# Performance work log

Measured on AMD Instinct MI355X. Metric: run time of the kernel, lower is better.

Reference implementation:

```python
import jax, jax.numpy as jnp
import numpy as np

N = 50000      # nodes
F_IN = 128     # num_feat
HID = 128      # hidden size
OUT = 47       # num_out (classes)
E = 600000     # graph edges
EGO_E = 1200000  # concatenated egonet edges


def _linear_params(key, fan_in, fan_out):
    s = 1.0 / np.sqrt(fan_in)
    kw, kb = jax.random.split(key)
    W = jax.random.uniform(kw, (fan_in, fan_out), jnp.float32, -s, s)
    b = jax.random.uniform(kb, (fan_out,), jnp.float32, -s, s)
    return W, b


def setup_inputs() -> dict:
    key = jax.random.key(0)
    ks = jax.random.split(key, 8)
    x_in = jax.random.normal(ks[0], (N, F_IN), jnp.float32)
    edge_index_in = jax.random.randint(ks[1], (2, E), 0, N)
    ego_edge_index = jax.random.randint(ks[2], (2, EGO_E), 0, N)
    W_ego0, b_ego0 = _linear_params(ks[3], F_IN, F_IN)
    W_gin0, b_gin0 = _linear_params(ks[4], F_IN, HID)
    W_ego1, b_ego1 = _linear_params(ks[5], HID, HID)
    W_gin1, b_gin1 = _linear_params(ks[6], HID, OUT)
    return {
        "x_in": x_in, "edge_index_in": edge_index_in, "ego_edge_index": ego_edge_index,
        "W_ego0": W_ego0, "b_ego0": b_ego0, "W_gin0": W_gin0, "b_gin0": b_gin0,
        "W_ego1": W_ego1, "b_ego1": b_ego1, "W_gin1": W_gin1, "b_gin1": b_gin1,
    }


def reference(x_in, edge_index_in, ego_edge_index,
              W_ego0, b_ego0, W_gin0, b_gin0,
              W_ego1, b_ego1, W_gin1, b_gin1):
    n = x_in.shape[0]
    ego_row, ego_col = ego_edge_index[0], ego_edge_index[1]
    src, tgt = edge_index_in[0], edge_index_in[1]

    def do_conv(x):
        # sum_i spmm(A_i, x) == scatter-add over concatenated egonet edges, then / N
        return jax.ops.segment_sum(x[ego_col], ego_row, num_segments=n) * (1.0 / n)

    def gin(x, W, b):
        # GINConv(nn=Linear), eps=0: Linear(x + sum_{j->i} x_j)
        aggr = jax.ops.segment_sum(x[src], tgt, num_segments=n)
        return (x + aggr) @ W + b

    # layer 0: ['Ego','GIN', relu_mid=True, relu_end=True]
    x = do_conv(x_in) @ W_ego0 + b_ego0
    x = jax.nn.relu(x)
    x = gin(x, W_gin0, b_gin0)
    x = jax.nn.relu(x)
    # layer 1: ['Ego','GIN', relu_mid=True, relu_end=False]
    x = do_conv(x) @ W_ego1 + b_ego1
    x = jax.nn.relu(x)
    x = gin(x, W_gin1, b_gin1)
    return jax.nn.log_softmax(x, axis=1)
```

## Files before the change

### kernel.cpp

```cpp
#include <hip/hip_runtime.h>

#define SCAP_EGO 8192
#define SCAP_E   4096

typedef unsigned short ushort_t;
typedef unsigned int uint_t;
typedef __attribute__((ext_vector_type(8))) short bf16x8;
typedef __attribute__((ext_vector_type(4))) float f32x4;

__device__ inline float lo16(uint_t u) { return __uint_as_float(u << 16); }
__device__ inline float hi16(uint_t u) { return __uint_as_float(u & 0xFFFF0000u); }
__device__ inline ushort_t f2bf(float f) {
    uint_t i = __float_as_uint(f);
    return (ushort_t)((i + 0x7FFFu + ((i >> 16) & 1u)) >> 16);
}
__device__ inline uint_t pack2(float a, float b) {
    return (uint_t)f2bf(a) | ((uint_t)f2bf(b) << 16);
}
union U8 { uint4 u; bf16x8 v; };

__global__ __launch_bounds__(256) void prep(
    const float* __restrict__ x, ushort_t* __restrict__ xb, int n8,
    const float* __restrict__ W0, const float* __restrict__ W1,
    const float* __restrict__ W2, const float* __restrict__ W3,
    ushort_t* __restrict__ T0, ushort_t* __restrict__ T1,
    ushort_t* __restrict__ T2, ushort_t* __restrict__ T3,
    int* __restrict__ z)
{
    int i = blockIdx.x * 256 + threadIdx.x;
    if (i < 128) ((int4*)z)[i] = make_int4(0, 0, 0, 0);
    if (i < n8) {
        const float4* p = (const float4*)(x + (size_t)i * 8);
        float4 a = p[0], b = p[1];
        uint4 o;
        o.x = pack2(a.x, a.y); o.y = pack2(a.z, a.w);
        o.z = pack2(b.x, b.y); o.w = pack2(b.z, b.w);
        *(uint4*)(xb + (size_t)i * 8) = o;
    }
    if (i < 49152) {
        int mi = i >> 14;
        int r = i & 16383;
        int n = r >> 7, k = r & 127;
        const float* W = mi == 0 ? W0 : (mi == 1 ? W1 : W2);
        ushort_t* T = mi == 0 ? T0 : (mi == 1 ? T1 : T2);
        T[n * 128 + k] = f2bf(W[k * 128 + n]);
    } else if (i < 49152 + 6144) {
        int r = i - 49152;
        int n = r >> 7, k = r & 127;
        T3[n * 128 + k] = (n < 47) ? f2bf(W3[k * 47 + n]) : (ushort_t)0;
    }
}

__global__ __launch_bounds__(256) void bin_edges2(
    const int* __restrict__ d1, const int* __restrict__ s1, int n1, int nb1,
    int* __restrict__ cur1, int2* __restrict__ st1, int scap1,
    const int* __restrict__ d2, const int* __restrict__ s2, int n2,
    int* __restrict__ cur2, int2* __restrict__ st2, int scap2)
{
    const int* dst; const int* src; int nE, scap; int* bincur; int2* stage; int bid;
    if (blockIdx.x < (uint_t)nb1) {
        dst = d1; src = s1; nE = n1; scap = scap1; bincur = cur1; stage = st1;
        bid = blockIdx.x;
    } else {
        dst = d2; src = s2; nE = n2; scap = scap2; bincur = cur2; stage = st2;
        bid = blockIdx.x - nb1;
    }
    __shared__ int bcnt[256];
    __shared__ int gbase[256];
    int t = threadIdx.x;
    bcnt[t] = 0;
    __syncthreads();
    int base = bid * 4096;
    int d[16], s[16], l[16];
#pragma unroll
    for (int i = 0; i < 16; i++) {
        int e = base + t + i * 256;
        if (e < nE) {
            d[i] = dst[e]; s[i] = src[e];
            l[i] = atomicAdd(&bcnt[d[i] >> 8], 1);
        } else d[i] = -1;
    }
    __syncthreads();
    if (bcnt[t]) gbase[t] = atomicAdd(&bincur[t], bcnt[t]);
    __syncthreads();
#pragma unroll
    for (int i = 0; i < 16; i++) {
        if (d[i] >= 0) {
            int b = d[i] >> 8;
            int slot = gbase[b] + l[i];
            if (slot < scap) stage[(size_t)b * scap + slot] = make_int2(d[i], s[i]);
        }
    }
}

__global__ __launch_bounds__(256) void build_csr2(
    const int* __restrict__ cur1, const int2* __restrict__ st1, int scap1,
    int* __restrict__ cnt1, int* __restrict__ rp1, int* __restrict__ pk1,
    const int* __restrict__ cur2, const int2* __restrict__ st2, int scap2,
    int* __restrict__ cnt2, int* __restrict__ rp2, int* __restrict__ pk2,
    int NB)
{
    const int* bincur; const int2* stage; int scap;
    int* cnt; int* rowptr; int* packed; int b;
    if (blockIdx.x < (uint_t)NB) {
        bincur = cur1; stage = st1; scap = scap1;
        cnt = cnt1; rowptr = rp1; packed = pk1; b = blockIdx.x;
    } else {
        bincur = cur2; stage = st2; scap = scap2;
        cnt = cnt2; rowptr = rp2; packed = pk2; b = blockIdx.x - NB;
    }
    __shared__ int sc[256];
    __shared__ int wcur[256];
    int t = threadIdx.x;
    int m = bincur[b]; if (m > scap) m = scap;
    const int2* st = stage + (size_t)b * scap;
    sc[t] = 0;
    __syncthreads();
    for (int e = t; e < m; e += 256) atomicAdd(&sc[st[e].x & 255], 1);
    __syncthreads();
    int v = sc[t];
    __syncthreads();
    sc[t] = v;
    __syncthreads();
    for (int off = 1; off < 256; off <<= 1) {
        int y = (t >= off) ? sc[t - off] : 0;
        __syncthreads();
        sc[t] += y;
        __syncthreads();
    }
    int excl = sc[t] - v;
    cnt[b * 256 + t] = v;
    rowptr[b * 256 + t] = b * scap + excl;
    wcur[t] = excl;
    __syncthreads();
    int* pk = packed + (size_t)b * scap;
    for (int e = t; e < m; e += 256) {
        int2 p = st[e];
        int slot = atomicAdd(&wcur[p.x & 255], 1);
        pk[slot] = p.y;
    }
}

__global__ __launch_bounds__(256) void gather_bf(
    const ushort_t* __restrict__ x, const int* __restrict__ cnt,
    const int* __restrict__ rowptr, const int* __restrict__ packed,
    ushort_t* __restrict__ outb, int nNodes, float scale, int selfAdd)
{
    int g = threadIdx.x >> 4, lane = threadIdx.x & 15;
    int n = blockIdx.x * 16 + g;
    if (n >= nNodes) return;
    int len = cnt[n];
    const int* row = packed + rowptr[n];
    const ushort_t* base = x + lane * 8;
    float a[8];
#pragma unroll
    for (int m = 0; m < 8; m++) a[m] = 0.f;
    int e = 0;
    for (; e + 3 < len; e += 4) {
        int s0 = row[e], s1 = row[e + 1], s2 = row[e + 2], s3 = row[e + 3];
        uint4 w0 = *(const uint4*)(base + (size_t)s0 * 128);
        uint4 w1 = *(const uint4*)(base + (size_t)s1 * 128);
        uint4 w2 = *(const uint4*)(base + (size_t)s2 * 128);
        uint4 w3 = *(const uint4*)(base + (size_t)s3 * 128);
        a[0] += lo16(w0.x) + lo16(w1.x) + lo16(w2.x) + lo16(w3.x);
        a[1] += hi16(w0.x) + hi16(w1.x) + hi16(w2.x) + hi16(w3.x);
        a[2] += lo16(w0.y) + lo16(w1.y) + lo16(w2.y) + lo16(w3.y);
        a[3] += hi16(w0.y) + hi16(w1.y) + hi16(w2.y) + hi16(w3.y);
        a[4] += lo16(w0.z) + lo16(w1.z) + lo16(w2.z) + lo16(w3.z);
        a[5] += hi16(w0.z) + hi16(w1.z) + hi16(w2.z) + hi16(w3.z);
        a[6] += lo16(w0.w) + lo16(w1.w) + lo16(w2.w) + lo16(w3.w);
        a[7] += hi16(w0.w) + hi16(w1.w) + hi16(w2.w) + hi16(w3.w);
    }
    for (; e < len; e++) {
        uint4 w = *(const uint4*)(base + (size_t)row[e] * 128);
        a[0] += lo16(w.x); a[1] += hi16(w.x);
        a[2] += lo16(w.y); a[3] += hi16(w.y);
        a[4] += lo16(w.z); a[5] += hi16(w.z);
        a[6] += lo16(w.w); a[7] += hi16(w.w);
    }
    if (selfAdd) {
        uint4 w = *(const uint4*)(base + (size_t)n * 128);
        a[0] += lo16(w.x); a[1] += hi16(w.x);
        a[2] += lo16(w.y); a[3] += hi16(w.y);
        a[4] += lo16(w.z); a[5] += hi16(w.z);
        a[6] += lo16(w.w); a[7] += hi16(w.w);
    }
    uint4 o;
    o.x = pack2(a[0] * scale, a[1] * scale);
    o.y = pack2(a[2] * scale, a[3] * scale);
    o.z = pack2(a[4] * scale, a[5] * scale);
    o.w = pack2(a[6] * scale, a[7] * scale);
    *(uint4*)(outb + (size_t)n * 128 + lane * 8) = o;
}

template<bool RELU>
__global__ __launch_bounds__(256) void gemm_mfma(
    const ushort_t* __restrict__ A, const ushort_t* __restrict__ WT,
    const float* __restrict__ bias, ushort_t* __restrict__ outb, int nrows)
{
    __shared__ ushort_t Ws[128][136];
    int t = threadIdx.x;
    for (int j = t; j < 128 * 16; j += 256) {
        int n = j >> 4, kq = (j & 15) << 3;
        *(uint4*)&Ws[n][kq] = *(const uint4*)(WT + n * 128 + kq);
    }
    int wave = t >> 6, lane = t & 63;
    int m = lane & 15, quad = lane >> 4;
    int rowBase = blockIdx.x * 64 + wave * 16;
    int arow = rowBase + m; if (arow >= nrows) arow = 0;
    bf16x8 afr[4];
#pragma unroll
    for (int kt = 0; kt < 4; kt++) {
        U8 u; u.u = *(const uint4*)(A + (size_t)arow * 128 + kt * 32 + quad * 8);
        afr[kt] = u.v;
    }
    __syncthreads();
    f32x4 acc[8];
#pragma unroll
    for (int ct = 0; ct < 8; ct++) acc[ct] = (f32x4){0.f, 0.f, 0.f, 0.f};
#pragma unroll
    for (int ct = 0; ct < 8; ct++) {
#pragma unroll
        for (int kt = 0; kt < 4; kt++) {
            bf16x8 b = *(const bf16x8*)&Ws[ct * 16 + m][kt * 32 + quad * 8];
            acc[ct] = __builtin_amdgcn_mfma_f32_16x16x32_bf16(afr[kt], b, acc[ct], 0, 0, 0);
        }
    }
#pragma unroll
    for (int ct = 0; ct < 8; ct++) {
        int col = ct * 16 + m;
        float bb = bias[col];
#pragma unroll
        for (int r = 0; r < 4; r++) {
            int row = rowBase + quad * 4 + r;
            if (row < nrows) {
                float v = acc[ct][r] + bb;
                if (RELU) v = fmaxf(v, 0.f);
                outb[(size_t)row * 128 + col] = f2bf(v);
            }
        }
    }
}

__global__ __launch_bounds__(256) void gemm47_lsm(
    const ushort_t* __restrict__ A, const ushort_t* __restrict__ WT,
    const float* __restrict__ bias, float* __restrict__ out, int nrows)
{
    __shared__ ushort_t Ws[48][136];
    int t = threadIdx.x;
    for (int j = t; j < 48 * 16; j += 256) {
        int n = j >> 4, kq = (j & 15) << 3;
        *(uint4*)&Ws[n][kq] = *(const uint4*)(WT + n * 128 + kq);
    }
    int wave = t >> 6, lane = t & 63;
    int m = lane & 15, quad = lane >> 4;
    int rowBase = blockIdx.x * 64 + wave * 16;
    int arow = rowBase + m; if (arow >= nrows) arow = 0;
    bf16x8 afr[4];
#pragma unroll
    for (int kt = 0; kt < 4; kt++) {
        U8 u; u.u = *(const uint4*)(A + (size_t)arow * 128 + kt * 32 + quad * 8);
        afr[kt] = u.v;
    }
    __syncthreads();
    f32x4 acc[3];
#pragma unroll
    for (int ct = 0; ct < 3; ct++) acc[ct] = (f32x4){0.f, 0.f, 0.f, 0.f};
#pragma unroll
    for (int ct = 0; ct < 3; ct++) {
#pragma unroll
        for (int kt = 0; kt < 4; kt++) {
            bf16x8 b = *(const bf16x8*)&Ws[ct * 16 + m][kt * 32 + quad * 8];
            acc[ct] = __builtin_amdgcn_mfma_f32_16x16x32_bf16(afr[kt], b, acc[ct], 0, 0, 0);
        }
    }
    int c0 = m, c1 = 16 + m, c2 = 32 + m;
    bool has2 = (c2 < 47);
    float b0 = bias[c0], b1 = bias[c1], b2 = has2 ? bias[c2] : 0.f;
#pragma unroll
    for (int r = 0; r < 4; r++) {
        int row = rowBase + quad * 4 + r;
        float v0 = acc[0][r] + b0;
        float v1 = acc[1][r] + b1;
        float v2 = has2 ? (acc[2][r] + b2) : -INFINITY;
        float mx = fmaxf(fmaxf(v0, v1), v2);
#pragma unroll
        for (int off = 8; off; off >>= 1) mx = fmaxf(mx, __shfl_xor(mx, off, 64));
        float s = __expf(v0 - mx) + __expf(v1 - mx) + (has2 ? __expf(v2 - mx) : 0.f);
#pragma unroll
        for (int off = 8; off; off >>= 1) s += __shfl_xor(s, off, 64);
        float lse = mx + __logf(s);
        if (row < nrows) {
            float* o = out + (size_t)row * 47;
            o[c0] = v0 - lse;
            o[c1] = v1 - lse;
            if (has2) o[c2] = v2 - lse;
        }
    }
}

extern "C" void kernel_launch(void* const* d_in, const int* in_sizes, int n_in,
                              void* d_out, int out_size, void* d_ws, size_t ws_size,
                              hipStream_t stream) {
    const float* x_in   = (const float*)d_in[0];
    const int*   edge   = (const int*)d_in[1];
    const int*   ego    = (const int*)d_in[2];
    const float* W_ego0 = (const float*)d_in[3];
    const float* b_ego0 = (const float*)d_in[4];
    const float* W_gin0 = (const float*)d_in[5];
    const float* b_gin0 = (const float*)d_in[6];
    const float* W_ego1 = (const float*)d_in[7];
    const float* b_ego1 = (const float*)d_in[8];
    const float* W_gin1 = (const float*)d_in[9];
    const float* b_gin1 = (const float*)d_in[10];
    float* out = (float*)d_out;

    const int N     = in_sizes[0] / 128;
    const int E     = in_sizes[1] / 2;
    const int EGO_E = in_sizes[2] / 2;
    const float invN = 1.0f / (float)N;
    const int NB    = (N + 255) >> 8;

    const size_t NBELEM = (size_t)N * 128;
    ushort_t* Xb = (ushort_t*)d_ws;
    ushort_t* G  = Xb + NBELEM;
    ushort_t* H  = G + NBELEM;
    ushort_t* T0 = H + NBELEM;
    ushort_t* T1 = T0 + 16384;
    ushort_t* T2 = T1 + 16384;
    ushort_t* T3 = T2 + 16384;
    int* ip = (int*)(T3 + 6144);
    int* cnt_ego   = ip;             ip += NB * 256;
    int* rp_ego    = ip;             ip += NB * 256;
    int* cnt_edge  = ip;             ip += NB * 256;
    int* rp_edge   = ip;             ip += NB * 256;
    int* bincur    = ip;             ip += 512;
    int2* stage_ego  = (int2*)ip;    ip += (size_t)NB * SCAP_EGO * 2;
    int*  pk_ego     = ip;           ip += (size_t)NB * SCAP_EGO;
    int2* stage_edge = (int2*)ip;    ip += (size_t)NB * SCAP_E * 2;
    int*  pk_edge    = ip;           ip += (size_t)NB * SCAP_E;

    const int gGemm   = (N + 63) / 64;
    const int gNode16 = (N + 15) / 16;
    const int gBinE   = (EGO_E + 4095) / 4096;
    const int gBinF   = (E + 4095) / 4096;
    const int gCvt    = ((N * 128 / 8) + 255) / 256;

    prep<<<gCvt, 256, 0, stream>>>(x_in, Xb, N * 128 / 8,
                                   W_ego0, W_gin0, W_ego1, W_gin1,
                                   T0, T1, T2, T3, bincur);
    bin_edges2<<<gBinE + gBinF, 256, 0, stream>>>(
        ego, ego + EGO_E, EGO_E, gBinE, bincur, stage_ego, SCAP_EGO,
        edge + E, edge, E, bincur + 256, stage_edge, SCAP_E);
    build_csr2<<<2 * NB, 256, 0, stream>>>(
        bincur, stage_ego, SCAP_EGO, cnt_ego, rp_ego, pk_ego,
        bincur + 256, stage_edge, SCAP_E, cnt_edge, rp_edge, pk_edge, NB);

    gather_bf<<<gNode16, 256, 0, stream>>>(Xb, cnt_ego, rp_ego, pk_ego, G, N, invN, 0);
    gemm_mfma<true><<<gGemm, 256, 0, stream>>>(G, T0, b_ego0, H, N);
    gather_bf<<<gNode16, 256, 0, stream>>>(H, cnt_edge, rp_edge, pk_edge, G, N, 1.f, 1);
    gemm_mfma<true><<<gGemm, 256, 0, stream>>>(G, T1, b_gin0, H, N);
    gather_bf<<<gNode16, 256, 0, stream>>>(H, cnt_ego, rp_ego, pk_ego, G, N, invN, 0);
    gemm_mfma<true><<<gGemm, 256, 0, stream>>>(G, T2, b_ego1, H, N);
    gather_bf<<<gNode16, 256, 0, stream>>>(H, cnt_edge, rp_edge, pk_edge, G, N, 1.f, 1);
    gemm47_lsm<<<gGemm, 256, 0, stream>>>(G, T3, b_gin1, out, N);
}
```

Baseline: 308.0 us.

## Fuse neighbor gather into MFMA GEMM kernels via LDS staging

Replaces separate gather and GEMM kernels with fused kernels that aggregate neighbor rows into a shared-memory tile and then run the MFMA matmul on it, removing the intermediate global write and read and half the launches. The gather now uses 32-bit per-lane loads across four column slices, re-reading edge indices per slice. This raises LDS usage, lowers occupancy, and issues more, narrower memory requests in exchange for the fusion.

```diff
diff --git a/kernel.cpp b/kernel.cpp
--- a/kernel.cpp
+++ b/kernel.cpp
@@ -141,80 +141,69 @@
     }
 }
 
-__global__ __launch_bounds__(256) void gather_bf(
-    const ushort_t* __restrict__ x, const int* __restrict__ cnt,
-    const int* __restrict__ rowptr, const int* __restrict__ packed,
-    ushort_t* __restrict__ outb, int nNodes, float scale, int selfAdd)
-{
-    int g = threadIdx.x >> 4, lane = threadIdx.x & 15;
-    int n = blockIdx.x * 16 + g;
-    if (n >= nNodes) return;
-    int len = cnt[n];
-    const int* row = packed + rowptr[n];
-    const ushort_t* base = x + lane * 8;
-    float a[8];
-#pragma unroll
-    for (int m = 0; m < 8; m++) a[m] = 0.f;
-    int e = 0;
-    for (; e + 3 < len; e += 4) {
-        int s0 = row[e], s1 = row[e + 1], s2 = row[e + 2], s3 = row[e + 3];
-        uint4 w0 = *(const uint4*)(base + (size_t)s0 * 128);
-        uint4 w1 = *(const uint4*)(base + (size_t)s1 * 128);
-        uint4 w2 = *(const uint4*)(base + (size_t)s2 * 128);
-        uint4 w3 = *(const uint4*)(base + (size_t)s3 * 128);
-        a[0] += lo16(w0.x) + lo16(w1.x) + lo16(w2.x) + lo16(w3.x);
-        a[1] += hi16(w0.x) + hi16(w1.x) + hi16(w2.x) + hi16(w3.x);
-        a[2] += lo16(w0.y) + lo16(w1.y) + lo16(w2.y) + lo16(w3.y);
-        a[3] += hi16(w0.y) + hi16(w1.y) + hi16(w2.y) + hi16(w3.y);
-        a[4] += lo16(w0.z) + lo16(w1.z) + lo16(w2.z) + lo16(w3.z);
-        a[5] += hi16(w0.z) + hi16(w1.z) + hi16(w2.z) + hi16(w3.z);
-        a[6] += lo16(w0.w) + lo16(w1.w) + lo16(w2.w) + lo16(w3.w);
-        a[7] += hi16(w0.w) + hi16(w1.w) + hi16(w2.w) + hi16(w3.w);
-    }
-    for (; e < len; e++) {
-        uint4 w = *(const uint4*)(base + (size_t)row[e] * 128);
-        a[0] += lo16(w.x); a[1] += hi16(w.x);
-        a[2] += lo16(w.y); a[3] += hi16(w.y);
-        a[4] += lo16(w.z); a[5] += hi16(w.z);
-        a[6] += lo16(w.w); a[7] += hi16(w.w);
-    }
-    if (selfAdd) {
-        uint4 w = *(const uint4*)(base + (size_t)n * 128);
-        a[0] += lo16(w.x); a[1] += hi16(w.x);
-        a[2] += lo16(w.y); a[3] += hi16(w.y);
-        a[4] += lo16(w.z); a[5] += hi16(w.z);
-        a[6] += lo16(w.w); a[7] += hi16(w.w);
-    }
-    uint4 o;
-    o.x = pack2(a[0] * scale, a[1] * scale);
-    o.y = pack2(a[2] * scale, a[3] * scale);
-    o.z = pack2(a[4] * scale, a[5] * scale);
-    o.w = pack2(a[6] * scale, a[7] * scale);
-    *(uint4*)(outb + (size_t)n * 128 + lane * 8) = o;
-}
-
-template<bool RELU>
-__global__ __launch_bounds__(256) void gemm_mfma(
-    const ushort_t* __restrict__ A, const ushort_t* __restrict__ WT,
-    const float* __restrict__ bias, ushort_t* __restrict__ outb, int nrows)
+template<int SELF>
+__global__ __launch_bounds__(256) void fused128(
+    const ushort_t* __restrict__ X,
+    const int* __restrict__ cnt, const int* __restrict__ rowptr,
+    const int* __restrict__ packed,
+    const ushort_t* __restrict__ WT, const float* __restrict__ bias,
+    ushort_t* __restrict__ outb, int nrows, float scale)
 {
     __shared__ ushort_t Ws[128][136];
+    __shared__ ushort_t As[64][136];
     int t = threadIdx.x;
     for (int j = t; j < 128 * 16; j += 256) {
-        int n = j >> 4, kq = (j & 15) << 3;
-        *(uint4*)&Ws[n][kq] = *(const uint4*)(WT + n * 128 + kq);
-    }
-    int wave = t >> 6, lane = t & 63;
-    int m = lane & 15, quad = lane >> 4;
-    int rowBase = blockIdx.x * 64 + wave * 16;
-    int arow = rowBase + m; if (arow >= nrows) arow = 0;
+        int nn = j >> 4, kq = (j & 15) << 3;
+        *(uint4*)&Ws[nn][kq] = *(const uint4*)(WT + nn * 128 + kq);
+    }
+    int g = t >> 4, lane = t & 15;
+    int blockBase = blockIdx.x * 64;
+    const uint_t* Xu = (const uint_t*)X;
+#pragma unroll
+    for (int sl = 0; sl < 4; sl++) {
+        const uint_t* base = Xu + sl * 16 + lane;
+        for (int q = 0; q < 4; q++) {
+            int r = q * 16 + g;
+            int n = blockBase + r;
+            float a0 = 0.f, a1 = 0.f;
+            if (n < nrows) {
+                int len = cnt[n];
+                const int* row = packed + rowptr[n];
+                int e = 0;
+                for (; e + 7 < len; e += 8) {
+                    uint_t w0 = base[row[e] * 64];
+                    uint_t w1 = base[row[e + 1] * 64];
+                    uint_t w2 = base[row[e + 2] * 64];
+                    uint_t w3 = base[row[e + 3] * 64];
+                    uint_t w4 = base[row[e + 4] * 64];
+                    uint_t w5 = base[row[e + 5] * 64];
+                    uint_t w6 = base[row[e + 6] * 64];
+                    uint_t w7 = base[row[e + 7] * 64];
+                    a0 += lo16(w0) + lo16(w1) + lo16(w2) + lo16(w3)
+                        + lo16(w4) + lo16(w5) + lo16(w6) + lo16(w7);
+                    a1 += hi16(w0) + hi16(w1) + hi16(w2) + hi16(w3)
+                        + hi16(w4) + hi16(w5) + hi16(w6) + hi16(w7);
+                }
+                for (; e < len; e++) {
+                    uint_t w = base[row[e] * 64];
+                    a0 += lo16(w); a1 += hi16(w);
+                }
+                if (SELF) {
+                    uint_t w = base[n * 64];
+                    a0 += lo16(w); a1 += hi16(w);
+                }
+            }
+            *(uint_t*)&As[r][sl * 32 + lane * 2] = pack2(a0 * scale, a1 * scale);
+        }
+    }
+    __syncthreads();
+    int wave = t >> 6, l64 = t & 63;
+    int m = l64 & 15, quad = l64 >> 4;
+    int rowBase = blockBase + wave * 16;
     bf16x8 afr[4];
 #pragma unroll
-    for (int kt = 0; kt < 4; kt++) {
-        U8 u; u.u = *(const uint4*)(A + (size_t)arow * 128 + kt * 32 + quad * 8);
-        afr[kt] = u.v;
-    }
-    __syncthreads();
+    for (int kt = 0; kt < 4; kt++)
+        afr[kt] = *(const bf16x8*)&As[wave * 16 + m][kt * 32 + quad * 8];
     f32x4 acc[8];
 #pragma unroll
     for (int ct = 0; ct < 8; ct++) acc[ct] = (f32x4){0.f, 0.f, 0.f, 0.f};
@@ -235,34 +224,73 @@
             int row = rowBase + quad * 4 + r;
             if (row < nrows) {
                 float v = acc[ct][r] + bb;
-                if (RELU) v = fmaxf(v, 0.f);
+                v = fmaxf(v, 0.f);
                 outb[(size_t)row * 128 + col] = f2bf(v);
             }
         }
     }
 }
 
-__global__ __launch_bounds__(256) void gemm47_lsm(
-    const ushort_t* __restrict__ A, const ushort_t* __restrict__ WT,
-    const float* __restrict__ bias, float* __restrict__ out, int nrows)
+__global__ __launch_bounds__(256) void fused47(
+    const ushort_t* __restrict__ X,
+    const int* __restrict__ cnt, const int* __restrict__ rowptr,
+    const int* __restrict__ packed,
+    const ushort_t* __restrict__ WT, const float* __restrict__ bias,
+    float* __restrict__ out, int nrows)
 {
     __shared__ ushort_t Ws[48][136];
+    __shared__ ushort_t As[64][136];
     int t = threadIdx.x;
     for (int j = t; j < 48 * 16; j += 256) {
-        int n = j >> 4, kq = (j & 15) << 3;
-        *(uint4*)&Ws[n][kq] = *(const uint4*)(WT + n * 128 + kq);
-    }
-    int wave = t >> 6, lane = t & 63;
-    int m = lane & 15, quad = lane >> 4;
-    int rowBase = blockIdx.x * 64 + wave * 16;
-    int arow = rowBase + m; if (arow >= nrows) arow = 0;
+        int nn = j >> 4, kq = (j & 15) << 3;
+        *(uint4*)&Ws[nn][kq] = *(const uint4*)(WT + nn * 128 + kq);
+    }
+    int g = t >> 4, lane = t & 15;
+    int blockBase = blockIdx.x * 64;
+    const uint_t* Xu = (const uint_t*)X;
+#pragma unroll
+    for (int sl = 0; sl < 4; sl++) {
+        const uint_t* base = Xu + sl * 16 + lane;
+        for (int q = 0; q < 4; q++) {
+            int r = q * 16 + g;
+            int n = blockBase + r;
+            float a0 = 0.f, a1 = 0.f;
+            if (n < nrows) {
+                int len = cnt[n];
+                const int* row = packed + rowptr[n];
+                int e = 0;
+                for (; e + 7 < len; e += 8) {
+                    uint_t w0 = base[row[e] * 64];
+                    uint_t w1 = base[row[e + 1] * 64];
+                    uint_t w2 = base[row[e + 2] * 64];
+                    uint_t w3 = base[row[e + 3] * 64];
+                    uint_t w4 = base[row[e + 4] * 64];
+                    uint_t w5 = base[row[e + 5] * 64];
+                    uint_t w6 = base[row[e + 6] * 64];
+                    uint_t w7 = base[row[e + 7] * 64];
+                    a0 += lo16(w0) + lo16(w1) + lo16(w2) + lo16(w3)
+                        + lo16(w4) + lo16(w5) + lo16(w6) + lo16(w7);
+                    a1 += hi16(w0) + hi16(w1) + hi16(w2) + hi16(w3)
+                        + hi16(w4) + hi16(w5) + hi16(w6) + hi16(w7);
+                }
+                for (; e < len; e++) {
+                    uint_t w = base[row[e] * 64];
+                    a0 += lo16(w); a1 += hi16(w);
+                }
+                uint_t w = base[n * 64];
+                a0 += lo16(w); a1 += hi16(w);
+            }
+            *(uint_t*)&As[r][sl * 32 + lane * 2] = pack2(a0, a1);
+        }
+    }
+    __syncthreads();
+    int wave = t >> 6, l64 = t & 63;
+    int m = l64 & 15, quad = l64 >> 4;
+    int rowBase = blockBase + wave * 16;
     bf16x8 afr[4];
 #pragma unroll
-    for (int kt = 0; kt < 4; kt++) {
-        U8 u; u.u = *(const uint4*)(A + (size_t)arow * 128 + kt * 32 + quad * 8);
-        afr[kt] = u.v;
-    }
-    __syncthreads();
+    for (int kt = 0; kt < 4; kt++)
+        afr[kt] = *(const bf16x8*)&As[wave * 16 + m][kt * 32 + quad * 8];
     f32x4 acc[3];
 #pragma unroll
     for (int ct = 0; ct < 3; ct++) acc[ct] = (f32x4){0.f, 0.f, 0.f, 0.f};
@@ -340,8 +368,7 @@
     int2* stage_edge = (int2*)ip;    ip += (size_t)NB * SCAP_E * 2;
     int*  pk_edge    = ip;           ip += (size_t)NB * SCAP_E;
 
-    const int gGemm   = (N + 63) / 64;
-    const int gNode16 = (N + 15) / 16;
+    const int gFused  = (N + 63) / 64;
     const int gBinE   = (EGO_E + 4095) / 4096;
     const int gBinF   = (E + 4095) / 4096;
     const int gCvt    = ((N * 128 / 8) + 255) / 256;
@@ -356,12 +383,12 @@
         bincur, stage_ego, SCAP_EGO, cnt_ego, rp_ego, pk_ego,
         bincur + 256, stage_edge, SCAP_E, cnt_edge, rp_edge, pk_edge, NB);
 
-    gather_bf<<<gNode16, 256, 0, stream>>>(Xb, cnt_ego, rp_ego, pk_ego, G, N, invN, 0);
-    gemm_mfma<true><<<gGemm, 256, 0, stream>>>(G, T0, b_ego0, H, N);
-    gather_bf<<<gNode16, 256, 0, stream>>>(H, cnt_edge, rp_edge, pk_edge, G, N, 1.f, 1);
-    gemm_mfma<true><<<gGemm, 256, 0, stream>>>(G, T1, b_gin0, H, N);
-    gather_bf<<<gNode16, 256, 0, stream>>>(H, cnt_ego, rp_ego, pk_ego, G, N, invN, 0);
-    gemm_mfma<true><<<gGemm, 256, 0, stream>>>(G, T2, b_ego1, H, N);
-    gather_bf<<<gNode16, 256, 0, stream>>>(H, cnt_edge, rp_edge, pk_edge, G, N, 1.f, 1);
-    gemm47_lsm<<<gGemm, 256, 0, stream>>>(G, T3, b_gin1, out, N);
-}
+    fused128<0><<<gFused, 256, 0, stream>>>(Xb, cnt_ego, rp_ego, pk_ego,
+                                            T0, b_ego0, H, N, invN);
+    fused128<1><<<gFused, 256, 0, stream>>>(H, cnt_edge, rp_edge, pk_edge,
+                                            T1, b_gin0, G, N, 1.f);
+    fused128<0><<<gFused, 256, 0, stream>>>(G, cnt_ego, rp_ego, pk_ego,
+                                            T2, b_ego1, H, N, invN);
+    fused47<<<gFused, 256, 0, stream>>>(H, cnt_edge, rp_edge, pk_edge,
+                                        T3, b_gin1, out, N);
+}
```

Result: slower. 706.0 us (+129.2%).

## Split gather feature dimension into four column slices across blocks

Applied to the files above, without the earlier changes.

The gather kernel now assigns each block one 32-column slice of 64 nodes, with 4 threads per node instead of 16. Each row gather then touches a 64-byte segment, and slices are spread across blocks, which is meant to raise concurrent nodes per wave and improve cache locality of each slice's working set. It also templates the self-add flag and sets launch bounds for higher occupancy. The trade-off is that the neighbor index lists are read four times, and each load covers a smaller contiguous chunk.

```diff
diff --git a/kernel.cpp b/kernel.cpp
--- a/kernel.cpp
+++ b/kernel.cpp
@@ -141,27 +141,30 @@
     }
 }
 
-__global__ __launch_bounds__(256) void gather_bf(
-    const ushort_t* __restrict__ x, const int* __restrict__ cnt,
-    const int* __restrict__ rowptr, const int* __restrict__ packed,
-    ushort_t* __restrict__ outb, int nNodes, float scale, int selfAdd)
-{
-    int g = threadIdx.x >> 4, lane = threadIdx.x & 15;
-    int n = blockIdx.x * 16 + g;
-    if (n >= nNodes) return;
+template<int SELF>
+__global__ __launch_bounds__(256, 8) void gatherS(
+    const ushort_t* __restrict__ X,
+    const int* __restrict__ cnt, const int* __restrict__ rowptr,
+    const int* __restrict__ packed,
+    ushort_t* __restrict__ outb, int nrows, float scale)
+{
+    int slice = blockIdx.x & 3;
+    int chunk = blockIdx.x >> 2;
+    int grp = threadIdx.x >> 2, lane = threadIdx.x & 3;
+    int n = chunk * 64 + grp;
+    if (n >= nrows) return;
+    const ushort_t* base = X + slice * 32 + lane * 8;
+    float a[8];
+#pragma unroll
+    for (int i = 0; i < 8; i++) a[i] = 0.f;
     int len = cnt[n];
     const int* row = packed + rowptr[n];
-    const ushort_t* base = x + lane * 8;
-    float a[8];
-#pragma unroll
-    for (int m = 0; m < 8; m++) a[m] = 0.f;
     int e = 0;
     for (; e + 3 < len; e += 4) {
-        int s0 = row[e], s1 = row[e + 1], s2 = row[e + 2], s3 = row[e + 3];
-        uint4 w0 = *(const uint4*)(base + (size_t)s0 * 128);
-        uint4 w1 = *(const uint4*)(base + (size_t)s1 * 128);
-        uint4 w2 = *(const uint4*)(base + (size_t)s2 * 128);
-        uint4 w3 = *(const uint4*)(base + (size_t)s3 * 128);
+        uint4 w0 = *(const uint4*)(base + (size_t)row[e] * 128);
+        uint4 w1 = *(const uint4*)(base + (size_t)row[e + 1] * 128);
+        uint4 w2 = *(const uint4*)(base + (size_t)row[e + 2] * 128);
+        uint4 w3 = *(const uint4*)(base + (size_t)row[e + 3] * 128);
         a[0] += lo16(w0.x) + lo16(w1.x) + lo16(w2.x) + lo16(w3.x);
         a[1] += hi16(w0.x) + hi16(w1.x) + hi16(w2.x) + hi16(w3.x);
         a[2] += lo16(w0.y) + lo16(w1.y) + lo16(w2.y) + lo16(w3.y);
@@ -178,7 +181,7 @@
         a[4] += lo16(w.z); a[5] += hi16(w.z);
         a[6] += lo16(w.w); a[7] += hi16(w.w);
     }
-    if (selfAdd) {
+    if (SELF) {
         uint4 w = *(const uint4*)(base + (size_t)n * 128);
         a[0] += lo16(w.x); a[1] += hi16(w.x);
         a[2] += lo16(w.y); a[3] += hi16(w.y);
@@ -190,7 +193,7 @@
     o.y = pack2(a[2] * scale, a[3] * scale);
     o.z = pack2(a[4] * scale, a[5] * scale);
     o.w = pack2(a[6] * scale, a[7] * scale);
-    *(uint4*)(outb + (size_t)n * 128 + lane * 8) = o;
+    *(uint4*)(outb + (size_t)n * 128 + slice * 32 + lane * 8) = o;
 }
 
 template<bool RELU>
@@ -340,8 +343,8 @@
     int2* stage_edge = (int2*)ip;    ip += (size_t)NB * SCAP_E * 2;
     int*  pk_edge    = ip;           ip += (size_t)NB * SCAP_E;
 
+    const int gSl     = 4 * ((N + 63) / 64);
     const int gGemm   = (N + 63) / 64;
-    const int gNode16 = (N + 15) / 16;
     const int gBinE   = (EGO_E + 4095) / 4096;
     const int gBinF   = (E + 4095) / 4096;
     const int gCvt    = ((N * 128 / 8) + 255) / 256;
@@ -356,12 +359,12 @@
         bincur, stage_ego, SCAP_EGO, cnt_ego, rp_ego, pk_ego,
         bincur + 256, stage_edge, SCAP_E, cnt_edge, rp_edge, pk_edge, NB);
 
-    gather_bf<<<gNode16, 256, 0, stream>>>(Xb, cnt_ego, rp_ego, pk_ego, G, N, invN, 0);
+    gatherS<0><<<gSl, 256, 0, stream>>>(Xb, cnt_ego, rp_ego, pk_ego, G, N, invN);
     gemm_mfma<true><<<gGemm, 256, 0, stream>>>(G, T0, b_ego0, H, N);
-    gather_bf<<<gNode16, 256, 0, stream>>>(H, cnt_edge, rp_edge, pk_edge, G, N, 1.f, 1);
+    gatherS<1><<<gSl, 256, 0, stream>>>(H, cnt_edge, rp_edge, pk_edge, G, N, 1.f);
     gemm_mfma<true><<<gGemm, 256, 0, stream>>>(G, T1, b_gin0, H, N);
-    gather_bf<<<gNode16, 256, 0, stream>>>(H, cnt_ego, rp_ego, pk_ego, G, N, invN, 0);
+    gatherS<0><<<gSl, 256, 0, stream>>>(H, cnt_ego, rp_ego, pk_ego, G, N, invN);
     gemm_mfma<true><<<gGemm, 256, 0, stream>>>(G, T2, b_ego1, H, N);
-    gather_bf<<<gNode16, 256, 0, stream>>>(H, cnt_edge, rp_edge, pk_edge, G, N, 1.f, 1);
+    gatherS<1><<<gSl, 256, 0, stream>>>(H, cnt_edge, rp_edge, pk_edge, G, N, 1.f);
     gemm47_lsm<<<gGemm, 256, 0, stream>>>(G, T3, b_gin1, out, N);
 }
```

Measured after the change: 374.9 us. 21.7% more time.
